# Kernel optimization log

Measured on AMD Instinct MI355X. Metric: run time of the kernel, lower is better.

## Reference

```python
import jax, jax.numpy as jnp
import numpy as np

D_MODEL = 1024
HEADS = 16
HEAD_DIM = D_MODEL // HEADS


def setup_inputs() -> dict:
    key = jax.random.key(0)
    ks = jax.random.split(key, 9)
    s = 1.0 / np.sqrt(D_MODEL)
    inp = {
        "inputs": jax.random.normal(ks[0], (4, 2048, D_MODEL), dtype=jnp.float32),
        "Wq": jax.random.normal(ks[1], (D_MODEL, D_MODEL), dtype=jnp.float32) * s,
        "bq": jnp.zeros((D_MODEL,), dtype=jnp.float32),
        "Wk": jax.random.normal(ks[2], (D_MODEL, D_MODEL), dtype=jnp.float32) * s,
        "bk": jnp.zeros((D_MODEL,), dtype=jnp.float32),
        "Wv": jax.random.normal(ks[3], (D_MODEL, D_MODEL), dtype=jnp.float32) * s,
        "bv": jnp.zeros((D_MODEL,), dtype=jnp.float32),
        "Wo": jax.random.normal(ks[4], (D_MODEL, D_MODEL), dtype=jnp.float32) * s,
        "bo": jnp.zeros((D_MODEL,), dtype=jnp.float32),
    }
    return inp


def reference(inputs, Wq, bq, Wk, bk, Wv, bv, Wo, bo):
    bs, seq, _ = inputs.shape
    # projections -> [b, h, s, d]
    def split_heads(x):
        return x.reshape(bs, seq, HEADS, HEAD_DIM).transpose(0, 2, 1, 3)
    q = split_heads(inputs @ Wq + bq)
    k = split_heads(inputs @ Wk + bk)
    v = split_heads(inputs @ Wv + bv)
    # NOTE: original code divides by (head_dim ** 1 / 2) == head_dim/2, not sqrt(head_dim)
    scale = HEAD_DIM / 2.0
    scores = jnp.einsum("bhqd,bhkd->bhqk", q, k) / scale
    attn = jax.nn.softmax(scores, axis=-1)
    out = jnp.einsum("bhqk,bhkd->bhqd", attn, v)
    out = out.transpose(0, 2, 1, 3).reshape(bs, seq, HEADS * HEAD_DIM)
    return out @ Wo + bo
```

## Files before the change

### kernel.cpp

```cpp
#include <hip/hip_runtime.h>
#include <stdint.h>

typedef __attribute__((ext_vector_type(8))) short bf16x8;
typedef __attribute__((ext_vector_type(4))) float f32x4;
typedef __attribute__((address_space(1))) void as1_void;
typedef __attribute__((address_space(3))) void as3_void;

#define D_MODEL 1024
#define SEQ     2048
#define BATCH   4
#define HEADS   16
#define HDIM    64

#define QSCALE 0.045084220029218407f

__device__ __forceinline__ ushort f2bf(float f) {
  union { float f; unsigned u; } v; v.f = f;
  unsigned u = v.u + 0x7fffu + ((v.u >> 16) & 1u);
  return (ushort)(u >> 16);
}

__device__ __forceinline__ void gload_lds16(const void* g, void* l) {
  __builtin_amdgcn_global_load_lds((as1_void*)(uintptr_t)g, (as3_void*)l, 16, 0, 0);
}

__device__ __forceinline__ bf16x8 pack8(float a0, float a1, float a2, float a3,
                                        float a4, float a5, float a6, float a7) {
  union { uint u[4]; bf16x8 v; } x;
  x.u[0] = __builtin_amdgcn_perm(__float_as_uint(a1), __float_as_uint(a0), 0x07060302);
  x.u[1] = __builtin_amdgcn_perm(__float_as_uint(a3), __float_as_uint(a2), 0x07060302);
  x.u[2] = __builtin_amdgcn_perm(__float_as_uint(a5), __float_as_uint(a4), 0x07060302);
  x.u[3] = __builtin_amdgcn_perm(__float_as_uint(a7), __float_as_uint(a6), 0x07060302);
  return x.v;
}

__global__ void prep_kernel(const float* __restrict__ X,
                            const float* w0, const float* w1, const float* w2, const float* w3,
                            const float* __restrict__ bq, const float* __restrict__ bk,
                            const float* __restrict__ bv,
                            ushort* __restrict__ Xb, ushort* __restrict__ WT,
                            float* __restrict__ bcat) {
  __shared__ float tile[32][33];
  const int bx = blockIdx.x, t = threadIdx.x;
  if (bx < 8192) {
    int i = bx * 256 + t;
    float4 f = reinterpret_cast<const float4*>(X)[i];
    ushort4 o;
    o.x = f2bf(f.x); o.y = f2bf(f.y); o.z = f2bf(f.z); o.w = f2bf(f.w);
    reinterpret_cast<ushort4*>(Xb)[i] = o;
  } else if (bx < 12288) {
    int tz = bx - 8192;
    int z = tz >> 10;
    int xy = tz & 1023;
    int bxt = xy & 31, byt = xy >> 5;
    const float* w = (z == 0) ? w0 : (z == 1) ? w1 : (z == 2) ? w2 : w3;
    const float sc = (z == 0) ? QSCALE : 1.0f;
    ushort* o = WT + (size_t)z * D_MODEL * D_MODEL;
    int tx = t & 31, ty = t >> 5;
    int x = bxt * 32 + tx;
    int y0 = byt * 32;
    #pragma unroll
    for (int i = ty; i < 32; i += 8)
      tile[i][tx] = w[(size_t)(y0 + i) * D_MODEL + x];
    __syncthreads();
    #pragma unroll
    for (int i = ty; i < 32; i += 8)
      o[(size_t)(bxt * 32 + i) * D_MODEL + y0 + tx] = f2bf(tile[tx][i] * sc);
  } else {
    int i = (bx - 12288) * 256 + t;
    bcat[i] = (i < 1024) ? bq[i] * QSCALE : (i < 2048) ? bk[i - 1024] : bv[i - 2048];
  }
}

#define MFMA16(a, b, c) __builtin_amdgcn_mfma_f32_16x16x32_bf16(a, b, c, 0, 0, 0)

template <int BN, bool F32OUT>
__global__ __launch_bounds__(256, 2) void gemm2p(const ushort* __restrict__ A,
                                                 const ushort* __restrict__ BT,
                                                 const float* __restrict__ bias,
                                                 ushort* __restrict__ QK,
                                                 ushort* __restrict__ Vt,
                                                 float* __restrict__ Cf) {
  static_assert(BN == 128, "gemm2p tuned for BN=128");
  constexpr int BB = BN * 128;
  __shared__ __align__(16) char smem[32768 + 2 * BB];
  const int tid  = threadIdx.x;
  const int w    = tid >> 6, lane = tid & 63;
  const int lo   = lane & 15, quad = lane >> 4;
  const int wr   = w >> 1, wc = w & 1;

  const int nx   = gridDim.x;
  const int nwg  = nx * gridDim.y;
  const int orig = blockIdx.y * nx + blockIdx.x;
  const int wg   = (orig & 7) * (nwg >> 3) + (orig >> 3);
  const int m0   = (wg / nx) * 128;
  const int n0   = (wg % nx) * BN;

  const int tl = tid ^ ((tid >> 3) & 7);
  const ushort* sA = A  + (size_t)(m0 + (tl >> 3)) * 1024 + (tl & 7) * 8;
  const ushort* sB = BT + (size_t)(n0 + (tl >> 3)) * 1024 + (tl & 7) * 8;
  char* lwA = smem + w * 1024;
  char* lwB = smem + 32768 + w * 1024;

  const int o0 = (quad * 16) ^ ((lo & 7) << 4);
  const int o1 = o0 ^ 64;
  const int rdA = (wr * 64 + lo) * 128;
  const int rdB = 32768 + (wc * 64 + lo) * 128;

  f32x4 acc[4][4];
  #pragma unroll
  for (int i = 0; i < 4; ++i)
    #pragma unroll
    for (int j = 0; j < 4; ++j) acc[i][j] = {0.f, 0.f, 0.f, 0.f};

  gload_lds16(sA,             lwA);
  gload_lds16(sA + 32 * 1024, lwA + 4096);
  gload_lds16(sA + 64 * 1024, lwA + 8192);
  gload_lds16(sA + 96 * 1024, lwA + 12288);
  gload_lds16(sB,             lwB);
  gload_lds16(sB + 64 * 1024, lwB + 8192);
  gload_lds16(sB + 32 * 1024, lwB + 4096);
  gload_lds16(sB + 96 * 1024, lwB + 12288);
  asm volatile("s_waitcnt vmcnt(2)" ::: "memory");
  __builtin_amdgcn_s_barrier();
  asm volatile("" ::: "memory");

  const char* L = smem;
  #pragma unroll 2
  for (int kt = 0; kt < 16; ++kt) {
    const int bA = (kt & 1) << 14;
    const int bB = (kt & 1) * BB;
    const int nA = bA ^ 16384;
    const int nB = bB ^ BB;
    const int kc = (kt + 1) * 64;
    const bool pf = kt < 15;
    bf16x8 af[4][2], bfr[2][2];

    #pragma unroll
    for (int mi = 0; mi < 4; ++mi) {
      af[mi][0] = *(const bf16x8*)(L + bA + rdA + mi * 2048 + o0);
      af[mi][1] = *(const bf16x8*)(L + bA + rdA + mi * 2048 + o1);
    }
    #pragma unroll
    for (int j = 0; j < 2; ++j) {
      bfr[j][0] = *(const bf16x8*)(L + bB + rdB + j * 2048 + o0);
      bfr[j][1] = *(const bf16x8*)(L + bB + rdB + j * 2048 + o1);
    }
    if (pf) {
      gload_lds16(sA + kc,             lwA + nA);
      gload_lds16(sA + 32 * 1024 + kc, lwA + nA + 4096);
      gload_lds16(sA + 64 * 1024 + kc, lwA + nA + 8192);
      gload_lds16(sA + 96 * 1024 + kc, lwA + nA + 12288);
      gload_lds16(sB + kc,             lwB + nB);
      gload_lds16(sB + 64 * 1024 + kc, lwB + nB + 8192);
    }
    asm volatile("s_waitcnt lgkmcnt(0)" ::: "memory");
    __builtin_amdgcn_sched_barrier(0);
    __builtin_amdgcn_s_setprio(1);
    #pragma unroll
    for (int ks = 0; ks < 2; ++ks)
      #pragma unroll
      for (int mi = 0; mi < 4; ++mi) {
        acc[mi][0] = MFMA16(af[mi][ks], bfr[0][ks], acc[mi][0]);
        acc[mi][1] = MFMA16(af[mi][ks], bfr[1][ks], acc[mi][1]);
      }
    __builtin_amdgcn_s_setprio(0);
    if (pf) asm volatile("s_waitcnt vmcnt(6)" ::: "memory");
    else    asm volatile("s_waitcnt vmcnt(0)" ::: "memory");
    __builtin_amdgcn_s_barrier();
    asm volatile("" ::: "memory");

    #pragma unroll
    for (int j = 0; j < 2; ++j) {
      bfr[j][0] = *(const bf16x8*)(L + bB + rdB + (2 + j) * 2048 + o0);
      bfr[j][1] = *(const bf16x8*)(L + bB + rdB + (2 + j) * 2048 + o1);
    }
    if (pf) {
      gload_lds16(sB + 32 * 1024 + kc, lwB + nB + 4096);
      gload_lds16(sB + 96 * 1024 + kc, lwB + nB + 12288);
    }
    asm volatile("s_waitcnt lgkmcnt(0)" ::: "memory");
    __builtin_amdgcn_sched_barrier(0);
    __builtin_amdgcn_s_setprio(1);
    #pragma unroll
    for (int ks = 0; ks < 2; ++ks)
      #pragma unroll
      for (int mi = 0; mi < 4; ++mi) {
        acc[mi][2] = MFMA16(af[mi][ks], bfr[0][ks], acc[mi][2]);
        acc[mi][3] = MFMA16(af[mi][ks], bfr[1][ks], acc[mi][3]);
      }
    __builtin_amdgcn_s_setprio(0);
    if (pf) {
      asm volatile("s_waitcnt vmcnt(2)" ::: "memory");
      __builtin_amdgcn_s_barrier();
      asm volatile("" ::: "memory");
    }
  }

  if constexpr (F32OUT) {
    #pragma unroll
    for (int ni = 0; ni < 4; ++ni) {
      const int col = n0 + wc * 64 + ni * 16 + lo;
      const float bv = bias[col];
      #pragma unroll
      for (int mi = 0; mi < 4; ++mi) {
        const int row = m0 + wr * 64 + mi * 16 + quad * 4;
        #pragma unroll
        for (int r = 0; r < 4; ++r)
          Cf[(size_t)(row + r) * 1024 + col] = acc[mi][ni][r] + bv;
      }
    }
  } else if (n0 < 2048) {
    #pragma unroll
    for (int ni = 0; ni < 4; ++ni) {
      const int col = n0 + wc * 64 + ni * 16 + lo;
      const float bv = bias[col];
      #pragma unroll
      for (int mi = 0; mi < 4; ++mi) {
        const int row = m0 + wr * 64 + mi * 16 + quad * 4;
        #pragma unroll
        for (int r = 0; r < 4; ++r)
          QK[(size_t)(row + r) * 2048 + col] = f2bf(acc[mi][ni][r] + bv);
      }
    }
  } else {
    #pragma unroll
    for (int ni = 0; ni < 4; ++ni) {
      const int col  = n0 + wc * 64 + ni * 16 + lo;
      const int vcol = col - 2048;
      const int hh = vcol >> 6, d = vcol & 63;
      const float bv = bias[col];
      #pragma unroll
      for (int mi = 0; mi < 4; ++mi) {
        const int base = m0 + wr * 64 + mi * 16;
        const int brow = base + quad * 4;
        const int bidx = brow >> 11;
        const int srow = brow & 2047;
        const int ck   = srow >> 6;
        const int c0   = (base & 32) + (quad << 3) + ((base >> 2) & 4);
        ushort e0 = f2bf(acc[mi][ni][0] + bv);
        ushort e1 = f2bf(acc[mi][ni][1] + bv);
        ushort e2 = f2bf(acc[mi][ni][2] + bv);
        ushort e3 = f2bf(acc[mi][ni][3] + bv);
        uint2 pk;
        pk.x = (uint)e0 | ((uint)e1 << 16);
        pk.y = (uint)e2 | ((uint)e3 << 16);
        *(uint2*)&Vt[(size_t)((bidx * HEADS + hh) * HDIM + d) * SEQ + ck * 64 + c0] = pk;
      }
    }
  }
}

__global__ __launch_bounds__(256, 2) void attn_kernel(const ushort* __restrict__ QK,
                                                      const ushort* __restrict__ Vt,
                                                      ushort* __restrict__ Og) {
  __shared__ __align__(16) ushort Ks[2][64 * 64];
  __shared__ __align__(16) ushort Vs[2][64 * 64];

  const int tid  = threadIdx.x;
  const int w    = tid >> 6, lane = tid & 63;
  const int lo   = lane & 15, quad = lane >> 4;

  const int p  = blockIdx.x + (blockIdx.y << 3) + (blockIdx.z << 7);
  const int G  = ((p >> 6) << 3) | (p & 7);
  const int h  = G & 15, b = G >> 4;
  const int qbase = ((p >> 3) & 7) * 256 + w * 64;
  const int swz = lo & 7;

  auto STAGE = [&](int buf, int ck) {
    #pragma unroll
    for (int i = 0; i < 2; ++i) {
      const int c16 = (w * 2 + i) * 64 + lane;
      const int r = c16 >> 3, ps = c16 & 7;
      const int gs = ps ^ (r & 7);
      gload_lds16(QK + (size_t)(b * SEQ + ck * 64 + r) * 2048 + 1024 + h * HDIM + gs * 8,
                  &Ks[buf][(w * 2 + i) * 512]);
      gload_lds16(Vt + (size_t)((b * HEADS + h) * HDIM + r) * SEQ + ck * 64 + gs * 8,
                  &Vs[buf][(w * 2 + i) * 512]);
    }
  };

  bf16x8 qf[4][2];
  #pragma unroll
  for (int qg = 0; qg < 4; ++qg) {
    const ushort* qp = QK + (size_t)(b * SEQ + qbase + qg * 16 + lo) * 2048 + h * HDIM;
    qf[qg][0] = *(const bf16x8*)(qp + quad * 8);
    qf[qg][1] = *(const bf16x8*)(qp + 32 + quad * 8);
  }

  f32x4 acc[4][4];
  #pragma unroll
  for (int qg = 0; qg < 4; ++qg)
    #pragma unroll
    for (int t = 0; t < 4; ++t) acc[qg][t] = {0.f, 0.f, 0.f, 0.f};
  float lsum[4] = {0.f, 0.f, 0.f, 0.f};

  STAGE(0, 0);
  __syncthreads();

  #pragma unroll 2
  for (int ck = 0; ck < SEQ / 64; ++ck) {
    const int cur = ck & 1;
    if (ck < SEQ / 64 - 1) {
      STAGE(cur ^ 1, ck + 1);
      asm volatile("s_waitcnt vmcnt(4)" ::: "memory");
    } else {
      asm volatile("s_waitcnt vmcnt(0)" ::: "memory");
    }
    __builtin_amdgcn_s_barrier();
    asm volatile("" ::: "memory");

    bf16x8 kf[4][2];
    #pragma unroll
    for (int sub = 0; sub < 4; ++sub) {
      const ushort* kr = &Ks[cur][(sub * 16 + lo) * 64];
      kf[sub][0] = *(const bf16x8*)(kr + ((quad ^ swz) * 8));
      kf[sub][1] = *(const bf16x8*)(kr + (((4 + quad) ^ swz) * 8));
    }

    bf16x8 af[4][2];
    #pragma unroll
    for (int qg = 0; qg < 4; ++qg) {
      f32x4 s[4];
      #pragma unroll
      for (int sub = 0; sub < 4; ++sub) s[sub] = {0.f, 0.f, 0.f, 0.f};
      #pragma unroll
      for (int sub = 0; sub < 4; ++sub) {
        s[sub] = __builtin_amdgcn_mfma_f32_16x16x32_bf16(kf[sub][0], qf[qg][0], s[sub], 0, 0, 0);
        s[sub] = __builtin_amdgcn_mfma_f32_16x16x32_bf16(kf[sub][1], qf[qg][1], s[sub], 0, 0, 0);
      }
      float p2[4][4];
      #pragma unroll
      for (int sub = 0; sub < 4; ++sub)
        #pragma unroll
        for (int r = 0; r < 4; ++r) p2[sub][r] = __builtin_amdgcn_exp2f(s[sub][r]);
      float t0 = 0.f;
      #pragma unroll
      for (int sub = 0; sub < 4; ++sub)
        t0 += (p2[sub][0] + p2[sub][1]) + (p2[sub][2] + p2[sub][3]);
      lsum[qg] += t0;
      af[qg][0] = pack8(p2[0][0], p2[0][1], p2[0][2], p2[0][3], p2[1][0], p2[1][1], p2[1][2], p2[1][3]);
      af[qg][1] = pack8(p2[2][0], p2[2][1], p2[2][2], p2[2][3], p2[3][0], p2[3][1], p2[3][2], p2[3][3]);
    }

    __builtin_amdgcn_s_setprio(1);
    #pragma unroll
    for (int t = 0; t < 4; ++t) {
      const ushort* vr = &Vs[cur][(t * 16 + lo) * 64];
      #pragma unroll
      for (int hh = 0; hh < 2; ++hh) {
        bf16x8 vf = *(const bf16x8*)(vr + (((hh * 4 + quad) ^ swz) * 8));
        #pragma unroll
        for (int qg = 0; qg < 4; ++qg)
          acc[qg][t] = __builtin_amdgcn_mfma_f32_16x16x32_bf16(af[qg][hh], vf, acc[qg][t], 0, 0, 0);
      }
    }
    __builtin_amdgcn_s_setprio(0);

    asm volatile("" ::: "memory");
    __builtin_amdgcn_s_barrier();
    asm volatile("" ::: "memory");
  }

  #pragma unroll
  for (int qg = 0; qg < 4; ++qg) {
    float v = lsum[qg];
    v += __shfl_xor(v, 16);
    v += __shfl_xor(v, 32);
    float linv[4];
    #pragma unroll
    for (int r = 0; r < 4; ++r) linv[r] = 1.0f / __shfl(v, quad * 4 + r);
    #pragma unroll
    for (int t = 0; t < 4; ++t)
      #pragma unroll
      for (int r = 0; r < 4; ++r)
        Og[(size_t)(b * SEQ + qbase + qg * 16 + quad * 4 + r) * D_MODEL + h * HDIM + t * 16 + lo] =
            f2bf(acc[qg][t][r] * linv[r]);
  }
}

extern "C" void kernel_launch(void* const* d_in, const int* in_sizes, int n_in,
                              void* d_out, int out_size, void* d_ws, size_t ws_size,
                              hipStream_t stream) {
  const float* X  = (const float*)d_in[0];
  const float* Wq = (const float*)d_in[1];
  const float* bq = (const float*)d_in[2];
  const float* Wk = (const float*)d_in[3];
  const float* bk = (const float*)d_in[4];
  const float* Wv = (const float*)d_in[5];
  const float* bv = (const float*)d_in[6];
  const float* Wo = (const float*)d_in[7];
  const float* bo = (const float*)d_in[8];
  float* out = (float*)d_out;
  char* ws = (char*)d_ws;

  ushort* Xb  = (ushort*)(ws);
  ushort* WT  = (ushort*)(ws + 16777216);
  ushort* QKb = (ushort*)(ws + 25165824);
  ushort* Vtb = (ushort*)(ws + 58720256);
  ushort* Ob  = (ushort*)(ws + 75497472);
  float*  bcat = (float*)(ws + 75497472);
  const int WSTRIDE = D_MODEL * D_MODEL;

  prep_kernel<<<12300, 256, 0, stream>>>(X, Wq, Wk, Wv, Wo, bq, bk, bv, Xb, WT, bcat);

  gemm2p<128, false><<<dim3(24, 64), 256, 0, stream>>>(Xb, WT, bcat, QKb, Vtb, nullptr);

  attn_kernel<<<dim3(SEQ / 256, HEADS, BATCH), 256, 0, stream>>>(QKb, Vtb, Ob);

  gemm2p<128, true><<<dim3(8, 64), 256, 0, stream>>>(Ob, WT + 3 * WSTRIDE, bo, nullptr, nullptr, out);
}
```

Measured before the change: 239.7 us.

## Process 128-key chunks per iteration and compute softmax row sums via MFMA

The attention loop now stages 128 keys per iteration instead of 64, which halves the number of barrier-separated iterations and doubles the LDS footprint per buffer. The per-lane float row-sum accumulation is replaced by an MFMA against a vector of bf16 ones, so the final shuffle reduction disappears and VALU adds move to the matrix unit. This raises LDS use and register pressure, which may hurt occupancy at two blocks per CU. It also sums the bf16-rounded probabilities rather than the fp32 values, which changes numerics slightly.

```diff
diff --git a/kernel.cpp b/kernel.cpp
--- a/kernel.cpp
+++ b/kernel.cpp
@@ -254,8 +254,8 @@
 __global__ __launch_bounds__(256, 2) void attn_kernel(const ushort* __restrict__ QK,
                                                       const ushort* __restrict__ Vt,
                                                       ushort* __restrict__ Og) {
-  __shared__ __align__(16) ushort Ks[2][64 * 64];
-  __shared__ __align__(16) ushort Vs[2][64 * 64];
+  __shared__ __align__(16) ushort Ks[2][128 * 64];
+  __shared__ __align__(16) ushort Vs[2][64 * 128];
 
   const int tid  = threadIdx.x;
   const int w    = tid >> 6, lane = tid & 63;
@@ -269,14 +269,17 @@
 
   auto STAGE = [&](int buf, int ck) {
     #pragma unroll
-    for (int i = 0; i < 2; ++i) {
-      const int c16 = (w * 2 + i) * 64 + lane;
-      const int r = c16 >> 3, ps = c16 & 7;
-      const int gs = ps ^ (r & 7);
-      gload_lds16(QK + (size_t)(b * SEQ + ck * 64 + r) * 2048 + 1024 + h * HDIM + gs * 8,
-                  &Ks[buf][(w * 2 + i) * 512]);
-      gload_lds16(Vt + (size_t)((b * HEADS + h) * HDIM + r) * SEQ + ck * 64 + gs * 8,
-                  &Vs[buf][(w * 2 + i) * 512]);
+    for (int i = 0; i < 4; ++i) {
+      const int seg = w * 4 + i;
+      const int c16 = seg * 64 + lane;
+      const int rK = c16 >> 3, pK = c16 & 7;
+      const int gK = pK ^ (rK & 7);
+      gload_lds16(QK + (size_t)(b * SEQ + ck * 128 + rK) * 2048 + 1024 + h * HDIM + gK * 8,
+                  &Ks[buf][seg * 512]);
+      const int rV = c16 >> 4, pV = c16 & 15;
+      const int gV = pV ^ (rV & 7);
+      gload_lds16(Vt + (size_t)((b * HEADS + h) * HDIM + rV) * SEQ + ck * 128 + gV * 8,
+                  &Vs[buf][seg * 512]);
     }
   };
 
@@ -288,71 +291,80 @@
     qf[qg][1] = *(const bf16x8*)(qp + 32 + quad * 8);
   }
 
-  f32x4 acc[4][4];
+  bf16x8 ones;
+  { union { uint u[4]; bf16x8 v; } o;
+    o.u[0] = o.u[1] = o.u[2] = o.u[3] = 0x3F803F80u; ones = o.v; }
+
+  f32x4 acc[4][4], acc_l[4];
   #pragma unroll
-  for (int qg = 0; qg < 4; ++qg)
+  for (int qg = 0; qg < 4; ++qg) {
+    acc_l[qg] = {0.f, 0.f, 0.f, 0.f};
     #pragma unroll
     for (int t = 0; t < 4; ++t) acc[qg][t] = {0.f, 0.f, 0.f, 0.f};
-  float lsum[4] = {0.f, 0.f, 0.f, 0.f};
+  }
 
   STAGE(0, 0);
   __syncthreads();
 
   #pragma unroll 2
-  for (int ck = 0; ck < SEQ / 64; ++ck) {
+  for (int ck = 0; ck < SEQ / 128; ++ck) {
     const int cur = ck & 1;
-    if (ck < SEQ / 64 - 1) {
+    if (ck < SEQ / 128 - 1) {
       STAGE(cur ^ 1, ck + 1);
-      asm volatile("s_waitcnt vmcnt(4)" ::: "memory");
+      asm volatile("s_waitcnt vmcnt(8)" ::: "memory");
     } else {
       asm volatile("s_waitcnt vmcnt(0)" ::: "memory");
     }
     __builtin_amdgcn_s_barrier();
     asm volatile("" ::: "memory");
 
-    bf16x8 kf[4][2];
-    #pragma unroll
-    for (int sub = 0; sub < 4; ++sub) {
-      const ushort* kr = &Ks[cur][(sub * 16 + lo) * 64];
-      kf[sub][0] = *(const bf16x8*)(kr + ((quad ^ swz) * 8));
-      kf[sub][1] = *(const bf16x8*)(kr + (((4 + quad) ^ swz) * 8));
-    }
-
-    bf16x8 af[4][2];
-    #pragma unroll
-    for (int qg = 0; qg < 4; ++qg) {
-      f32x4 s[4];
-      #pragma unroll
-      for (int sub = 0; sub < 4; ++sub) s[sub] = {0.f, 0.f, 0.f, 0.f};
-      #pragma unroll
-      for (int sub = 0; sub < 4; ++sub) {
-        s[sub] = __builtin_amdgcn_mfma_f32_16x16x32_bf16(kf[sub][0], qf[qg][0], s[sub], 0, 0, 0);
-        s[sub] = __builtin_amdgcn_mfma_f32_16x16x32_bf16(kf[sub][1], qf[qg][1], s[sub], 0, 0, 0);
-      }
-      float p2[4][4];
-      #pragma unroll
-      for (int sub = 0; sub < 4; ++sub)
-        #pragma unroll
-        for (int r = 0; r < 4; ++r) p2[sub][r] = __builtin_amdgcn_exp2f(s[sub][r]);
-      float t0 = 0.f;
-      #pragma unroll
-      for (int sub = 0; sub < 4; ++sub)
-        t0 += (p2[sub][0] + p2[sub][1]) + (p2[sub][2] + p2[sub][3]);
-      lsum[qg] += t0;
-      af[qg][0] = pack8(p2[0][0], p2[0][1], p2[0][2], p2[0][3], p2[1][0], p2[1][1], p2[1][2], p2[1][3]);
-      af[qg][1] = pack8(p2[2][0], p2[2][1], p2[2][2], p2[2][3], p2[3][0], p2[3][1], p2[3][2], p2[3][3]);
+    bf16x8 af[4][4];
+    #pragma unroll
+    for (int half = 0; half < 2; ++half) {
+      bf16x8 kf[4][2];
+      #pragma unroll
+      for (int s2 = 0; s2 < 4; ++s2) {
+        const ushort* kr = &Ks[cur][((half * 4 + s2) * 16 + lo) * 64];
+        kf[s2][0] = *(const bf16x8*)(kr + ((quad ^ swz) * 8));
+        kf[s2][1] = *(const bf16x8*)(kr + (((4 + quad) ^ swz) * 8));
+      }
+      #pragma unroll
+      for (int qg = 0; qg < 4; ++qg) {
+        f32x4 s[4];
+        #pragma unroll
+        for (int s2 = 0; s2 < 4; ++s2) s[s2] = {0.f, 0.f, 0.f, 0.f};
+        #pragma unroll
+        for (int s2 = 0; s2 < 4; ++s2) {
+          s[s2] = MFMA16(kf[s2][0], qf[qg][0], s[s2]);
+          s[s2] = MFMA16(kf[s2][1], qf[qg][1], s[s2]);
+        }
+        float p2[4][4];
+        #pragma unroll
+        for (int s2 = 0; s2 < 4; ++s2)
+          #pragma unroll
+          for (int r = 0; r < 4; ++r) p2[s2][r] = __builtin_amdgcn_exp2f(s[s2][r]);
+        af[qg][half * 2 + 0] = pack8(p2[0][0], p2[0][1], p2[0][2], p2[0][3],
+                                     p2[1][0], p2[1][1], p2[1][2], p2[1][3]);
+        af[qg][half * 2 + 1] = pack8(p2[2][0], p2[2][1], p2[2][2], p2[2][3],
+                                     p2[3][0], p2[3][1], p2[3][2], p2[3][3]);
+      }
     }
 
     __builtin_amdgcn_s_setprio(1);
     #pragma unroll
+    for (int qg = 0; qg < 4; ++qg)
+      #pragma unroll
+      for (int hh = 0; hh < 4; ++hh)
+        acc_l[qg] = MFMA16(af[qg][hh], ones, acc_l[qg]);
+    #pragma unroll
     for (int t = 0; t < 4; ++t) {
-      const ushort* vr = &Vs[cur][(t * 16 + lo) * 64];
-      #pragma unroll
-      for (int hh = 0; hh < 2; ++hh) {
+      const ushort* vr = &Vs[cur][(t * 16 + lo) * 128];
+      #pragma unroll
+      for (int hh = 0; hh < 4; ++hh) {
         bf16x8 vf = *(const bf16x8*)(vr + (((hh * 4 + quad) ^ swz) * 8));
         #pragma unroll
         for (int qg = 0; qg < 4; ++qg)
-          acc[qg][t] = __builtin_amdgcn_mfma_f32_16x16x32_bf16(af[qg][hh], vf, acc[qg][t], 0, 0, 0);
+          acc[qg][t] = MFMA16(af[qg][hh], vf, acc[qg][t]);
       }
     }
     __builtin_amdgcn_s_setprio(0);
@@ -364,12 +376,9 @@
 
   #pragma unroll
   for (int qg = 0; qg < 4; ++qg) {
-    float v = lsum[qg];
-    v += __shfl_xor(v, 16);
-    v += __shfl_xor(v, 32);
     float linv[4];
     #pragma unroll
-    for (int r = 0; r < 4; ++r) linv[r] = 1.0f / __shfl(v, quad * 4 + r);
+    for (int r = 0; r < 4; ++r) linv[r] = 1.0f / acc_l[qg][r];
     #pragma unroll
     for (int t = 0; t < 4; ++t)
       #pragma unroll
```

New measurement: 241.2 us. Within noise of the previous version (+0.6%).
